# Performance work log

Measured on AMD Instinct MI355X. Metric: run time of the kernel, lower is better.

## Reference

```python
import jax, jax.numpy as jnp
import numpy as np

IN_F, OUT_F = 8192, 8192
BETA, THRESHOLD, RESET = 0.99, 1.0, 0.8
TAU_POS, TAU_NEG = 20.0, 20.0
A_POS, A_NEG = 0.005, 0.005


def setup_inputs() -> dict:
    key = jax.random.key(0)
    k1, k2, k3, k4, k5 = jax.random.split(key, 5)
    in_spikes = (jax.random.uniform(k1, (IN_F,)) < 0.1).astype(jnp.float32)  # 0/1 spikes
    weights = jax.random.normal(k2, (OUT_F, IN_F), dtype=jnp.float32) * 0.02  # nn.Linear weight [out,in]
    membrane = jax.random.uniform(k3, (OUT_F,), dtype=jnp.float32)
    delta_pre = jax.random.randint(k4, (IN_F,), 0, 50).astype(jnp.float32)   # steps since last pre spike
    delta_fire = jax.random.randint(k5, (OUT_F,), 0, 50).astype(jnp.float32) # steps since last post spike
    return {"in_spikes": in_spikes, "weights": weights, "membrane": membrane,
            "delta_pre": delta_pre, "delta_fire": delta_fire}


def reference(in_spikes, weights, membrane, delta_pre, delta_fire):
    # GEVM: torch.mm(in_spikes[None], W.T).squeeze() == W @ in_spikes -> [OUT_F]
    weighted = weights @ in_spikes
    # LIF neuron
    mem = membrane * BETA + weighted
    out_spikes = (mem > THRESHOLD).astype(jnp.float32)
    new_membrane = jnp.where(out_spikes > 0, mem - RESET, mem)
    # delta counters: increment, reset to 0 where a spike occurred
    new_delta_pre = jnp.where(in_spikes > 0, 0.0, delta_pre + 1.0)
    new_delta_fire = jnp.where(out_spikes > 0, 0.0, delta_fire + 1.0)
    # outer-product timing difference [OUT_F, IN_F]
    delta_t = new_delta_fire[:, None] - new_delta_pre[None, :]
    potentiation = jnp.where(delta_t > 0, A_POS * jnp.exp(-delta_t / TAU_POS), 0.0)
    depression = jnp.where(delta_t < 0, A_NEG * jnp.exp(delta_t / TAU_NEG), 0.0)
    weight_changes = potentiation - depression
    new_weights = weights + weight_changes
    return out_spikes, new_membrane, new_delta_pre, new_delta_fire, new_weights
```

## Files before the change

kernel.cpp:

```cpp
#include <hip/hip_runtime.h>


#define IN_F 8192
#define OUT_F 8192

__constant__ const float kBeta = 0.99f;
__constant__ const float kThresh = 1.0f;
__constant__ const float kReset = 0.8f;
__constant__ const float kInvTau = 1.0f / 20.0f;
__constant__ const float kApos = 0.005f;
__constant__ const float kAneg = 0.005f;

__global__ void ndp_kernel(const float* __restrict__ in_spikes,
                           const float* __restrict__ delta_pre,
                           float* __restrict__ out_ndp) {
    int i = blockIdx.x * blockDim.x + threadIdx.x;
    if (i < IN_F) {
        out_ndp[i] = (in_spikes[i] > 0.0f) ? 0.0f : delta_pre[i] + 1.0f;
    }
}

__global__ __launch_bounds__(256) void row_kernel(
    const float* __restrict__ in_spikes,
    const float* __restrict__ W,
    const float* __restrict__ membrane,
    const float* __restrict__ delta_fire,
    const float* ndp,
    float* out)
{
    const int row = blockIdx.x;
    const int t   = threadIdx.x;
    const float* wrow = W + (size_t)row * IN_F;

    float4 w[8];
    float acc = 0.0f;
#pragma unroll
    for (int k = 0; k < 8; ++k) {
        const int c = k * 1024 + t * 4;
        w[k] = *(const float4*)(wrow + c);
        const float4 s = *(const float4*)(in_spikes + c);
        acc += w[k].x * s.x + w[k].y * s.y + w[k].z * s.z + w[k].w * s.w;
    }

    for (int off = 32; off > 0; off >>= 1) acc += __shfl_down(acc, off, 64);

    __shared__ float red[4];
    __shared__ float lut[51];
    __shared__ float s_ndf;
    const int wave = t >> 6;
    if ((t & 63) == 0) red[wave] = acc;
    __syncthreads();

    if (t == 0) {
        const float weighted = red[0] + red[1] + red[2] + red[3];
        const float mem   = membrane[row] * kBeta + weighted;
        const float spike = (mem > kThresh) ? 1.0f : 0.0f;
        const float nmem  = (spike > 0.0f) ? (mem - kReset) : mem;
        const float ndf   = (spike > 0.0f) ? 0.0f : (delta_fire[row] + 1.0f);
        out[row]             = spike;
        out[OUT_F + row]     = nmem;
        out[3 * OUT_F + row] = ndf;
        s_ndf = ndf;
    }
    __syncthreads();

    if (t < 51) {
        const float dt = s_ndf - (float)t;
        float ch;
        if (dt > 0.0f)      ch =  kApos * expf(-dt * kInvTau);
        else if (dt < 0.0f) ch = -kAneg * expf( dt * kInvTau);
        else                ch = 0.0f;
        lut[t] = ch;
    }
    __syncthreads();

    float* orow = out + 4 * OUT_F + (size_t)row * IN_F;
#pragma unroll
    for (int k = 0; k < 8; ++k) {
        const int c = k * 1024 + t * 4;
        const float4 p = *(const float4*)(ndp + c);
        float4 r;
        r.x = w[k].x + lut[(int)p.x];
        r.y = w[k].y + lut[(int)p.y];
        r.z = w[k].z + lut[(int)p.z];
        r.w = w[k].w + lut[(int)p.w];
        *(float4*)(orow + c) = r;
    }
}

extern "C" void kernel_launch(void* const* d_in, const int* in_sizes, int n_in,
                              void* d_out, int out_size, void* d_ws, size_t ws_size,
                              hipStream_t stream) {
    const float* in_spikes  = (const float*)d_in[0];
    const float* weights    = (const float*)d_in[1];
    const float* membrane   = (const float*)d_in[2];
    const float* delta_pre  = (const float*)d_in[3];
    const float* delta_fire = (const float*)d_in[4];
    float* out = (float*)d_out;

    float* out_ndp = out + 2 * OUT_F;

    ndp_kernel<<<(IN_F + 255) / 256, 256, 0, stream>>>(in_spikes, delta_pre, out_ndp);
    row_kernel<<<OUT_F, 256, 0, stream>>>(in_spikes, weights, membrane, delta_fire,
                                          out_ndp, out);
}
```

Measured before the change: 443.9 us.

## Fuse delta_pre kernel into row kernel with packed byte indices and nontemporal IO

Removes the separate ndp kernel launch. Each block now recomputes the new delta_pre indices from in_spikes and delta_pre and packs them as bytes into registers, and row 0 writes the ndp output. Weight loads and output stores use nontemporal builtins to avoid polluting cache with the 256MB+256MB stream. The LUT build now runs in parallel with the LIF scalar update, removing one barrier. It assumes delta_pre+1 fits in a byte (max 50), which holds for the stated input range.

```diff
diff --git a/kernel.cpp b/kernel.cpp
--- a/kernel.cpp
+++ b/kernel.cpp
@@ -4,73 +4,70 @@
 #define IN_F 8192
 #define OUT_F 8192
 
-__constant__ const float kBeta = 0.99f;
-__constant__ const float kThresh = 1.0f;
-__constant__ const float kReset = 0.8f;
-__constant__ const float kInvTau = 1.0f / 20.0f;
-__constant__ const float kApos = 0.005f;
-__constant__ const float kAneg = 0.005f;
+typedef float v4f __attribute__((ext_vector_type(4)));
 
-__global__ void ndp_kernel(const float* __restrict__ in_spikes,
-                           const float* __restrict__ delta_pre,
-                           float* __restrict__ out_ndp) {
-    int i = blockIdx.x * blockDim.x + threadIdx.x;
-    if (i < IN_F) {
-        out_ndp[i] = (in_spikes[i] > 0.0f) ? 0.0f : delta_pre[i] + 1.0f;
-    }
-}
-
-__global__ __launch_bounds__(256) void row_kernel(
+__global__ __launch_bounds__(256) void stdp_fused(
     const float* __restrict__ in_spikes,
     const float* __restrict__ W,
     const float* __restrict__ membrane,
+    const float* __restrict__ delta_pre,
     const float* __restrict__ delta_fire,
-    const float* ndp,
-    float* out)
+    float* __restrict__ out)
 {
+    constexpr float kBeta   = 0.99f;
+    constexpr float kThresh = 1.0f;
+    constexpr float kReset  = 0.8f;
+    constexpr float kInvTau = 1.0f / 20.0f;
+    constexpr float kA      = 0.005f;
+
     const int row = blockIdx.x;
     const int t   = threadIdx.x;
+
+    const float mrow  = membrane[row];
+    const float dfrow = delta_fire[row];
+
     const float* wrow = W + (size_t)row * IN_F;
 
-    float4 w[8];
+    v4f w[8];
+    unsigned int packed[8];
     float acc = 0.0f;
 #pragma unroll
     for (int k = 0; k < 8; ++k) {
         const int c = k * 1024 + t * 4;
-        w[k] = *(const float4*)(wrow + c);
-        const float4 s = *(const float4*)(in_spikes + c);
+        w[k] = __builtin_nontemporal_load((const v4f*)(wrow + c));
+        const v4f s  = *(const v4f*)(in_spikes + c);
+        const v4f dp = *(const v4f*)(delta_pre + c);
         acc += w[k].x * s.x + w[k].y * s.y + w[k].z * s.z + w[k].w * s.w;
+        const unsigned i0 = (s.x > 0.0f) ? 0u : (unsigned)(dp.x + 1.0f);
+        const unsigned i1 = (s.y > 0.0f) ? 0u : (unsigned)(dp.y + 1.0f);
+        const unsigned i2 = (s.z > 0.0f) ? 0u : (unsigned)(dp.z + 1.0f);
+        const unsigned i3 = (s.w > 0.0f) ? 0u : (unsigned)(dp.w + 1.0f);
+        packed[k] = i0 | (i1 << 8) | (i2 << 16) | (i3 << 24);
     }
 
+#pragma unroll
     for (int off = 32; off > 0; off >>= 1) acc += __shfl_down(acc, off, 64);
 
     __shared__ float red[4];
-    __shared__ float lut[51];
-    __shared__ float s_ndf;
-    const int wave = t >> 6;
-    if ((t & 63) == 0) red[wave] = acc;
-    __syncthreads();
-
-    if (t == 0) {
-        const float weighted = red[0] + red[1] + red[2] + red[3];
-        const float mem   = membrane[row] * kBeta + weighted;
-        const float spike = (mem > kThresh) ? 1.0f : 0.0f;
-        const float nmem  = (spike > 0.0f) ? (mem - kReset) : mem;
-        const float ndf   = (spike > 0.0f) ? 0.0f : (delta_fire[row] + 1.0f);
-        out[row]             = spike;
-        out[OUT_F + row]     = nmem;
-        out[3 * OUT_F + row] = ndf;
-        s_ndf = ndf;
-    }
+    __shared__ float lut[64];
+    if ((t & 63) == 0) red[t >> 6] = acc;
     __syncthreads();
 
     if (t < 51) {
-        const float dt = s_ndf - (float)t;
-        float ch;
-        if (dt > 0.0f)      ch =  kApos * expf(-dt * kInvTau);
-        else if (dt < 0.0f) ch = -kAneg * expf( dt * kInvTau);
-        else                ch = 0.0f;
+        const float weighted = red[0] + red[1] + red[2] + red[3];
+        const float mem   = mrow * kBeta + weighted;
+        const bool  fired = mem > kThresh;
+        const float ndf   = fired ? 0.0f : (dfrow + 1.0f);
+        const float dt    = ndf - (float)t;
+        float ch = 0.0f;
+        if (dt > 0.0f)      ch =  kA * expf(-dt * kInvTau);
+        else if (dt < 0.0f) ch = -kA * expf( dt * kInvTau);
         lut[t] = ch;
+        if (t == 0) {
+            out[row]             = fired ? 1.0f : 0.0f;
+            out[OUT_F + row]     = fired ? (mem - kReset) : mem;
+            out[3 * OUT_F + row] = ndf;
+        }
     }
     __syncthreads();
 
@@ -78,13 +75,28 @@
 #pragma unroll
     for (int k = 0; k < 8; ++k) {
         const int c = k * 1024 + t * 4;
-        const float4 p = *(const float4*)(ndp + c);
-        float4 r;
-        r.x = w[k].x + lut[(int)p.x];
-        r.y = w[k].y + lut[(int)p.y];
-        r.z = w[k].z + lut[(int)p.z];
-        r.w = w[k].w + lut[(int)p.w];
-        *(float4*)(orow + c) = r;
+        const unsigned p = packed[k];
+        v4f r;
+        r.x = w[k].x + lut[p & 0xffu];
+        r.y = w[k].y + lut[(p >> 8) & 0xffu];
+        r.z = w[k].z + lut[(p >> 16) & 0xffu];
+        r.w = w[k].w + lut[p >> 24];
+        __builtin_nontemporal_store(r, (v4f*)(orow + c));
+    }
+
+    if (row == 0) {
+        float* ondp = out + 2 * OUT_F;
+#pragma unroll
+        for (int k = 0; k < 8; ++k) {
+            const int c = k * 1024 + t * 4;
+            const unsigned p = packed[k];
+            v4f r;
+            r.x = (float)(p & 0xffu);
+            r.y = (float)((p >> 8) & 0xffu);
+            r.z = (float)((p >> 16) & 0xffu);
+            r.w = (float)(p >> 24);
+            *(v4f*)(ondp + c) = r;
+        }
     }
 }
 
@@ -98,9 +110,6 @@
     const float* delta_fire = (const float*)d_in[4];
     float* out = (float*)d_out;
 
-    float* out_ndp = out + 2 * OUT_F;
-
-    ndp_kernel<<<(IN_F + 255) / 256, 256, 0, stream>>>(in_spikes, delta_pre, out_ndp);
-    row_kernel<<<OUT_F, 256, 0, stream>>>(in_spikes, weights, membrane, delta_fire,
-                                          out_ndp, out);
+    stdp_fused<<<OUT_F, 256, 0, stream>>>(in_spikes, weights, membrane,
+                                          delta_pre, delta_fire, out);
 }
```

Measured after the change: 436.8 us. About the same (-1.6%).
